# Kernel optimization log

Hardware: AMD Instinct MI355X
Metric: run time of the kernel (lower is better)

The kernel has to match this reference:

```python
import jax, jax.numpy as jnp
import numpy as np

B, N, L, E, H, D = 2, 2048, 2048, 512, 8, 3
C = E // H
ALPHA_Q = 10.0

def _ln(v, g, b):
    m = jnp.mean(v, -1, keepdims=True)
    var = jnp.mean((v - m) ** 2, -1, keepdims=True)
    return (v - m) * jax.lax.rsqrt(var + 1e-5) * g + b

def setup_inputs() -> dict:
    key = jax.random.key(0)
    ks = jax.random.split(key, 16)
    def nrm(k, shape):
        return jax.random.normal(k, shape, jnp.float32) * 0.02
    return dict(
        x=jax.random.normal(ks[0], (B, N, E), jnp.float32),
        xp=jax.random.normal(ks[1], (B, N, D), jnp.float32),
        y=jax.random.normal(ks[2], (B, L, E), jnp.float32),
        yp=jax.random.normal(ks[3], (B, L, D), jnp.float32),
        attn_mask=jnp.ones((B, 1, N, L), jnp.float32),
        pW1=jax.random.uniform(ks[4], (E, D), jnp.float32, -1.0 / D, 1.0 / D),
        pb1=jax.random.uniform(ks[5], (E,), jnp.float32, 0.0, np.pi),
        pW2=jax.random.uniform(ks[6], (E, D), jnp.float32, -1.0 / D, 1.0 / D),
        pb2=jax.random.uniform(ks[7], (E,), jnp.float32, 0.0, np.pi),
        qn_g=jnp.ones((E,), jnp.float32), qn_b=jnp.zeros((E,), jnp.float32),
        qW1=nrm(ks[8], (E, E)), qb1=jnp.zeros((E,), jnp.float32),
        qW2=nrm(ks[9], (E, E)), qb2=jnp.zeros((E,), jnp.float32),
        kn_g=jnp.ones((E,), jnp.float32), kn_b=jnp.zeros((E,), jnp.float32),
        kW1=nrm(ks[10], (E, E)), kb1=jnp.zeros((E,), jnp.float32),
        vn_g=jnp.ones((E,), jnp.float32), vn_b=jnp.zeros((E,), jnp.float32),
        vW=nrm(ks[11], (E, E)), vb=jnp.zeros((E,), jnp.float32),
        p1W=nrm(ks[12], (E, E)), p1b=jnp.zeros((E,), jnp.float32),
        p2W=nrm(ks[13], (E, D * H)), p2b=jnp.zeros((E,), jnp.float32),
    )

def reference(x, xp, y, yp, attn_mask, pW1, pb1, pW2, pb2,
              qn_g, qn_b, qW1, qb1, qW2, qb2, kn_g, kn_b, kW1, kb1,
              vn_g, vn_b, vW, vb, p1W, p1b, p2W, p2b):
    # PositionEncoder: query side with bias, key side without
    pxs = ALPHA_Q * xp
    px1 = pxs @ pW1.T + pb1
    px2 = pxs @ pW2.T + pb2
    xc1, xs1, xc2, xs2 = jnp.cos(px1), jnp.sin(px1), jnp.cos(px2), jnp.sin(px2)
    pys = ALPHA_Q * yp
    py1 = pys @ pW1.T
    py2 = pys @ pW2.T
    yc1, ys1, yc2, ys2 = jnp.cos(py1), jnp.sin(py1), jnp.cos(py2), jnp.sin(py2)

    def split(t):  # [B,S,E] -> [B,S,H,C]
        return t.reshape(t.shape[0], t.shape[1], H, C)

    # QueryEncoder
    xn = _ln(x, qn_g, qn_b)
    x1 = xn @ qW1.T + qb1
    x2 = xn @ qW2.T + qb2
    q = jnp.concatenate([split(x1 * xc1), split(x1 * xs1),
                         split(x2 * xc2), split(x2 * xs2)], -1)  # [B,N,H,4C]
    q = q.transpose(0, 2, 1, 3)  # [B,H,N,4C]
    # KeyEncoder
    yn = _ln(y, kn_g, kn_b)
    y1 = yn @ kW1.T + kb1
    k = jnp.concatenate([split(y1 * yc1), split(y1 * ys1),
                         split(yc2), split(ys2)], -1).transpose(0, 2, 1, 3)

    scale = (4 * C) ** -0.5
    attn = jax.nn.softmax(jnp.einsum('bhnd,bhld->bhnl', q, k) * scale, axis=-1)
    # custom mask renormalization
    attn = attn * attn_mask
    eps = min(1e-8, 1.0 / L)
    attn = attn / (jnp.sum(attn, -1, keepdims=True) + eps)

    v = (_ln(y, vn_g, vn_b) @ vW.T + vb).reshape(B, L, H, C).transpose(0, 2, 1, 3)
    out1 = jnp.einsum('bhnl,bhlc->bhnc', attn, v).transpose(0, 2, 1, 3).reshape(B, N, E)
    out1 = out1 @ p1W.T + p1b

    out2 = jnp.einsum('bhnl,bld->bhnd', attn, yp) - xp[:, None]  # [B,H,N,D]
    out2 = out2.transpose(0, 2, 1, 3).reshape(B, N, H * D) @ p2W.T + p2b
    return (out1 + out2, attn)
```

## Files before the change

kernel.cpp:

```cpp
#include <hip/hip_runtime.h>

typedef unsigned short ushort_t;
typedef __attribute__((ext_vector_type(8))) __bf16 bf16x8;
typedef __attribute__((ext_vector_type(4))) float f32x4;

__device__ __forceinline__ f32x4 mfma16(bf16x8 a, bf16x8 b, f32x4 c) {
  return __builtin_amdgcn_mfma_f32_16x16x32_bf16(a, b, c, 0, 0, 0);
}

__device__ __forceinline__ ushort_t f2bf(float f) {
  unsigned int x = __float_as_uint(f);
  unsigned int r = (x + 0x7fffu + ((x >> 16) & 1u)) >> 16;
  return (ushort_t)r;
}

static constexpr size_t SZ_XN   = 4096ull * 512 * 2;
static constexpr size_t SZ_W    = 512ull * 512 * 2;
static constexpr size_t OFS_XN   = 0;
static constexpr size_t OFS_YNK  = OFS_XN + SZ_XN;
static constexpr size_t OFS_YNV  = OFS_YNK + SZ_XN;
static constexpr size_t OFS_WQ12 = OFS_YNV + SZ_XN;
static constexpr size_t OFS_WK1  = OFS_WQ12 + 2 * SZ_W;
static constexpr size_t OFS_WV   = OFS_WK1 + SZ_W;
static constexpr size_t OFS_WP1  = OFS_WV + SZ_W;
static constexpr size_t OFS_QB12 = OFS_WP1 + SZ_W;
static constexpr size_t OFS_FLAG = OFS_QB12 + 4096;
static constexpr size_t OFS_X12  = OFS_FLAG + 256;
static constexpr size_t OFS_INV  = OFS_X12;
static constexpr size_t OFS_Y1   = OFS_X12 + 4096ull * 1024 * 4;
static constexpr size_t OFS_VV   = OFS_Y1 + 4096ull * 512 * 4;
static constexpr size_t OFS_Q    = OFS_VV + 4096ull * 512 * 4;
static constexpr size_t OFS_K    = OFS_Q + 16ull * 2048 * 256 * 2;
static constexpr size_t OFS_VT   = OFS_K + 16ull * 2048 * 256 * 2;
static constexpr size_t OFS_O1   = OFS_VT + 16ull * 80 * 2048 * 2;
static constexpr size_t OFS_O2   = OFS_O1 + 4096ull * 512 * 2;
static constexpr size_t OFS_T    = OFS_O2 + 4096ull * 24 * 4;

__global__ void k_convert(const float* __restrict__ qW1, const float* __restrict__ qW2,
                          const float* __restrict__ kW1, const float* __restrict__ vW,
                          const float* __restrict__ p1W,
                          const float* __restrict__ qb1, const float* __restrict__ qb2,
                          ushort_t* wq12, ushort_t* wk1, ushort_t* wv, ushort_t* wp1,
                          float* qb12, int* flag) {
  int seg = blockIdx.y;
  int idx = blockIdx.x * 256 + threadIdx.x;
  switch (seg) {
    case 0: wq12[idx] = f2bf(qW1[idx]);
            if (idx < 512) qb12[idx] = qb1[idx];
            if (idx == 0) *flag = 1;
            break;
    case 1: wq12[262144 + idx] = f2bf(qW2[idx]);
            if (idx < 512) qb12[512 + idx] = qb2[idx];
            break;
    case 2: wk1[idx] = f2bf(kW1[idx]); break;
    case 3: wv[idx]  = f2bf(vW[idx]);  break;
    case 4: wp1[idx] = f2bf(p1W[idx]); break;
  }
}

__global__ void k_maskchk(const float4* __restrict__ mask, int* flag, int n4) {
  int i = blockIdx.x * blockDim.x + threadIdx.x;
  bool bad = false;
  for (; i < n4; i += gridDim.x * blockDim.x) {
    float4 v = mask[i];
    bad |= (v.x != 1.f) | (v.y != 1.f) | (v.z != 1.f) | (v.w != 1.f);
  }
  if (bad) atomicAnd(flag, 0);
}

__global__ __launch_bounds__(256) void k_ln1(const float* __restrict__ x,
                                             const float* __restrict__ g, const float* __restrict__ b,
                                             ushort_t* __restrict__ out) {
  int row = blockIdx.x, tid = threadIdx.x;
  const float* xr = x + (size_t)row * 512;
  float v0 = xr[tid], v1 = xr[tid + 256];
  float s = v0 + v1, q = v0 * v0 + v1 * v1;
  for (int m = 32; m; m >>= 1) { s += __shfl_xor(s, m, 64); q += __shfl_xor(q, m, 64); }
  __shared__ float ls[8];
  int wid = tid >> 6, lane = tid & 63;
  if (lane == 0) { ls[wid] = s; ls[4 + wid] = q; }
  __syncthreads();
  s = ls[0] + ls[1] + ls[2] + ls[3];
  q = ls[4] + ls[5] + ls[6] + ls[7];
  float mean = s * (1.f / 512), var = q * (1.f / 512) - mean * mean;
  float rs = rsqrtf(var + 1e-5f);
  ushort_t* o = out + (size_t)row * 512;
  o[tid]       = f2bf((v0 - mean) * rs * g[tid] + b[tid]);
  o[tid + 256] = f2bf((v1 - mean) * rs * g[tid + 256] + b[tid + 256]);
}

__global__ __launch_bounds__(256) void k_ln2(const float* __restrict__ y,
                                             const float* __restrict__ g1, const float* __restrict__ b1,
                                             const float* __restrict__ g2, const float* __restrict__ b2,
                                             ushort_t* __restrict__ o1, ushort_t* __restrict__ o2) {
  int row = blockIdx.x, tid = threadIdx.x;
  const float* yr = y + (size_t)row * 512;
  float v0 = yr[tid], v1 = yr[tid + 256];
  float s = v0 + v1, q = v0 * v0 + v1 * v1;
  for (int m = 32; m; m >>= 1) { s += __shfl_xor(s, m, 64); q += __shfl_xor(q, m, 64); }
  __shared__ float ls[8];
  int wid = tid >> 6, lane = tid & 63;
  if (lane == 0) { ls[wid] = s; ls[4 + wid] = q; }
  __syncthreads();
  s = ls[0] + ls[1] + ls[2] + ls[3];
  q = ls[4] + ls[5] + ls[6] + ls[7];
  float mean = s * (1.f / 512), var = q * (1.f / 512) - mean * mean;
  float rs = rsqrtf(var + 1e-5f);
  float t0 = (v0 - mean) * rs, t1 = (v1 - mean) * rs;
  ushort_t* p1 = o1 + (size_t)row * 512;
  ushort_t* p2 = o2 + (size_t)row * 512;
  p1[tid]       = f2bf(t0 * g1[tid] + b1[tid]);
  p1[tid + 256] = f2bf(t1 * g1[tid + 256] + b1[tid + 256]);
  p2[tid]       = f2bf(t0 * g2[tid] + b2[tid]);
  p2[tid + 256] = f2bf(t1 * g2[tid + 256] + b2[tid + 256]);
}

__global__ __launch_bounds__(256) void k_gemm(const ushort_t* __restrict__ A, const ushort_t* __restrict__ W,
                                              const float* __restrict__ bias, float* __restrict__ Cmat,
                                              int M, int Nn, int K, int mode,
                                              const float* __restrict__ o2, const float* __restrict__ p2W,
                                              const float* __restrict__ p2b) {
  __shared__ __align__(16) ushort_t lA[128 * 40];
  __shared__ __align__(16) ushort_t lB[128 * 40];
  int tid = threadIdx.x;
  int wid = tid >> 6, lane = tid & 63, lg = lane >> 4, lc = lane & 15;
  int m0 = blockIdx.y * 128, n0 = blockIdx.x * 128;
  int wm = wid >> 1, wn = wid & 1;
  f32x4 acc[4][4];
#pragma unroll
  for (int i = 0; i < 4; i++)
#pragma unroll
    for (int j = 0; j < 4; j++) acc[i][j] = (f32x4){0, 0, 0, 0};

  for (int k0 = 0; k0 < K; k0 += 32) {
    __syncthreads();
#pragma unroll
    for (int i = 0; i < 2; i++) {
      int u = tid + i * 256;
      int row = u >> 2, off = u & 3;
      *(int4*)(&lA[row * 40 + off * 8]) = *(const int4*)(A + (size_t)(m0 + row) * K + k0 + off * 8);
      *(int4*)(&lB[row * 40 + off * 8]) = *(const int4*)(W + (size_t)(n0 + row) * K + k0 + off * 8);
    }
    __syncthreads();
    bf16x8 af[4], bf[4];
#pragma unroll
    for (int mt = 0; mt < 4; mt++) af[mt] = *(const bf16x8*)(&lA[(wm * 64 + mt * 16 + lc) * 40 + lg * 8]);
#pragma unroll
    for (int nt = 0; nt < 4; nt++) bf[nt] = *(const bf16x8*)(&lB[(wn * 64 + nt * 16 + lc) * 40 + lg * 8]);
#pragma unroll
    for (int mt = 0; mt < 4; mt++)
#pragma unroll
      for (int nt = 0; nt < 4; nt++) acc[mt][nt] = mfma16(af[mt], bf[nt], acc[mt][nt]);
  }

#pragma unroll
  for (int mt = 0; mt < 4; mt++) {
#pragma unroll
    for (int nt = 0; nt < 4; nt++) {
      int col = n0 + wn * 64 + nt * 16 + lc;
      float bcol = bias[col];
#pragma unroll
      for (int r = 0; r < 4; r++) {
        int row = m0 + wm * 64 + mt * 16 + lg * 4 + r;
        float v = acc[mt][nt][r] + bcol;
        if (mode == 1) {
          const float* o2r = o2 + (size_t)row * 24;
          const float* wr = p2W + (size_t)col * 24;
          float sdot = p2b[col];
#pragma unroll
          for (int j = 0; j < 24; j++) sdot += o2r[j] * wr[j];
          v += sdot;
        }
        Cmat[(size_t)row * Nn + col] = v;
      }
    }
  }
}

__global__ __launch_bounds__(256) void k_scatter_q(const float* __restrict__ x12, const float* __restrict__ xp,
                                                   const float* __restrict__ pW1, const float* __restrict__ pb1,
                                                   const float* __restrict__ pW2, const float* __restrict__ pb2,
                                                   ushort_t* __restrict__ q) {
  int rown = blockIdx.x;
  int b = rown >> 11, n = rown & 2047;
  float p0 = xp[(size_t)rown * 3] * 10.f;
  float p1 = xp[(size_t)rown * 3 + 1] * 10.f;
  float p2v = xp[(size_t)rown * 3 + 2] * 10.f;
  const float* x1r = x12 + (size_t)rown * 1024;
#pragma unroll
  for (int i = 0; i < 2; i++) {
    int e = threadIdx.x + i * 256;
    float a1 = p0 * pW1[e * 3] + p1 * pW1[e * 3 + 1] + p2v * pW1[e * 3 + 2] + pb1[e];
    float a2 = p0 * pW2[e * 3] + p1 * pW2[e * 3 + 1] + p2v * pW2[e * 3 + 2] + pb2[e];
    float c1, s1, c2, s2;
    __sincosf(a1, &s1, &c1);
    __sincosf(a2, &s2, &c2);
    float x1 = x1r[e], x2 = x1r[512 + e];
    int h = e >> 6, c = e & 63;
    ushort_t* qr = q + (((size_t)b * 8 + h) * 2048 + n) * 256;
    qr[c]       = f2bf(x1 * c1);
    qr[64 + c]  = f2bf(x1 * s1);
    qr[128 + c] = f2bf(x2 * c2);
    qr[192 + c] = f2bf(x2 * s2);
  }
}

__global__ __launch_bounds__(256) void k_scatter_k(const float* __restrict__ y1, const float* __restrict__ yp,
                                                   const float* __restrict__ pW1, const float* __restrict__ pW2,
                                                   ushort_t* __restrict__ kk) {
  int rown = blockIdx.x;
  int b = rown >> 11, n = rown & 2047;
  float p0 = yp[(size_t)rown * 3] * 10.f;
  float p1 = yp[(size_t)rown * 3 + 1] * 10.f;
  float p2v = yp[(size_t)rown * 3 + 2] * 10.f;
  const float* y1r = y1 + (size_t)rown * 512;
#pragma unroll
  for (int i = 0; i < 2; i++) {
    int e = threadIdx.x + i * 256;
    float a1 = p0 * pW1[e * 3] + p1 * pW1[e * 3 + 1] + p2v * pW1[e * 3 + 2];
    float a2 = p0 * pW2[e * 3] + p1 * pW2[e * 3 + 1] + p2v * pW2[e * 3 + 2];
    float c1, s1, c2, s2;
    __sincosf(a1, &s1, &c1);
    __sincosf(a2, &s2, &c2);
    float v1 = y1r[e];
    int h = e >> 6, c = e & 63;
    ushort_t* kr = kk + (((size_t)b * 8 + h) * 2048 + n) * 256;
    kr[c]       = f2bf(v1 * c1);
    kr[64 + c]  = f2bf(v1 * s1);
    kr[128 + c] = f2bf(c2);
    kr[192 + c] = f2bf(s2);
  }
}

__global__ void k_vt(const float* __restrict__ vv, ushort_t* __restrict__ vt) {
  int l0 = blockIdx.x * 64, h = blockIdx.y, b = blockIdx.z;
  __shared__ ushort_t t[64][66];
  int tx = threadIdx.x, ty = threadIdx.y;
#pragma unroll
  for (int i = 0; i < 16; i++) {
    int lr = i * 4 + ty;
    t[lr][tx] = f2bf(vv[((size_t)(b * 2048 + l0 + lr)) * 512 + h * 64 + tx]);
  }
  __syncthreads();
#pragma unroll
  for (int i = 0; i < 16; i++) {
    int col = i * 4 + ty;
    vt[(((size_t)b * 8 + h) * 80 + col) * 2048 + l0 + tx] = t[tx][col];
  }
}

__global__ void k_vt_extra(const float* __restrict__ yp, ushort_t* __restrict__ vt) {
  int l = blockIdx.x * 256 + threadIdx.x;
  int j = blockIdx.y, bh = blockIdx.z;
  int b = bh >> 3;
  ushort_t v = 0;
  if (j < 3) v = f2bf(yp[((size_t)b * 2048 + l) * 3 + j]);
  vt[((size_t)bh * 80 + 64 + j) * 2048 + l] = v;
}

__global__ __launch_bounds__(256, 2) void k_attn1(const ushort_t* __restrict__ qbuf,
                                                  const ushort_t* __restrict__ kbuf,
                                                  const ushort_t* __restrict__ vt,
                                                  const float* __restrict__ mask,
                                                  const int* __restrict__ flag,
                                                  const float* __restrict__ xp,
                                                  float* __restrict__ invb,
                                                  ushort_t* __restrict__ Tb,
                                                  ushort_t* __restrict__ o1,
                                                  float* __restrict__ o2) {
  __shared__ __align__(16) ushort_t kL[2][32 * 256];
  __shared__ __align__(16) ushort_t aT[4][16][40];

  int flat = blockIdx.x;
  int bh = flat & 15, rb = flat >> 4;
  int b = bh >> 3, h = bh & 7;
  int tid = threadIdx.x, wid = tid >> 6, lane = tid & 63, lg = lane >> 4, lc = lane & 15;
  int wrow = rb * 64 + wid * 16;
  const bool ones = (*flag != 0);

  const ushort_t* Kb = kbuf + (size_t)bh * 2048 * 256;
  const ushort_t* Vb = vt + (size_t)bh * 80 * 2048;
  ushort_t* Trow = Tb + ((size_t)bh * 2048 + wrow + lc) * 2048 + lg * 8;

  bf16x8 qf[8];
  {
    const ushort_t* qr = qbuf + ((size_t)bh * 2048 + wrow + lc) * 256 + lg * 8;
#pragma unroll
    for (int ks = 0; ks < 8; ks++) qf[ks] = *(const bf16x8*)(qr + ks * 32);
  }

  int sg_src[4], sg_dst[4];
#pragma unroll
  for (int i = 0; i < 4; i++) {
    int g = wid * 256 + i * 64 + lane;
    int row = g >> 5;
    int gc = (g & 31) ^ (row & 7);
    sg_src[i] = row * 256 + gc * 8;
    sg_dst[i] = (wid * 256 + i * 64) * 8;
  }

#define STAGE(s, t)                                                                     \
  {                                                                                     \
    const ushort_t* tb = Kb + (size_t)(t) * 32 * 256;                                   \
    _Pragma("unroll")                                                                   \
    for (int i = 0; i < 4; i++) {                                                       \
      __builtin_amdgcn_global_load_lds(                                                 \
          (const __attribute__((address_space(1))) void*)(tb + sg_src[i]),              \
          (__attribute__((address_space(3))) void*)(&kL[s][sg_dst[i]]), 16, 0, 0);      \
    }                                                                                   \
  }

  int r3 = (lc & 7);

  float rsE[4] = {0, 0, 0, 0}, rsM[4] = {0, 0, 0, 0};
  f32x4 pacc[5];
#pragma unroll
  for (int nt = 0; nt < 5; nt++) pacc[nt] = (f32x4){0, 0, 0, 0};

  STAGE(0, 0);
  asm volatile("s_waitcnt vmcnt(0)" ::: "memory");
  __builtin_amdgcn_s_barrier();
  __builtin_amdgcn_sched_barrier(0);

  for (int t = 0; t < 64; t++) {
    int s = t & 1;
    int l0 = t * 32;
    if (t < 63) { STAGE(s ^ 1, t + 1); }
    bf16x8 vf[5];
#pragma unroll
    for (int nt = 0; nt < 5; nt++)
      vf[nt] = *(const bf16x8*)(Vb + (size_t)(nt * 16 + lc) * 2048 + l0 + lg * 8);
    __builtin_amdgcn_sched_barrier(0);
    f32x4 sacc[2];
    sacc[0] = (f32x4){0, 0, 0, 0};
    sacc[1] = (f32x4){0, 0, 0, 0};
#pragma unroll
    for (int ks = 0; ks < 8; ks++) {
      int gb = ((ks * 4 + lg) ^ r3) * 8;
      bf16x8 k0 = *(const bf16x8*)(&kL[s][lc * 256 + gb]);
      bf16x8 k1 = *(const bf16x8*)(&kL[s][(16 + lc) * 256 + gb]);
      sacc[0] = mfma16(qf[ks], k0, sacc[0]);
      sacc[1] = mfma16(qf[ks], k1, sacc[1]);
    }
#pragma unroll
    for (int nt = 0; nt < 2; nt++)
#pragma unroll
      for (int r = 0; r < 4; r++) {
        float T = __expf(sacc[nt][r] * 0.0625f);
        rsE[r] += T;
        float Tm = T;
        if (!ones) {
          float m = mask[((size_t)b * 2048 + wrow + lg * 4 + r) * 2048 + l0 + nt * 16 + lc];
          Tm = T * m;
          rsM[r] += Tm;
        }
        aT[wid][lg * 4 + r][nt * 16 + lc] = f2bf(Tm);
      }
    asm volatile("s_waitcnt lgkmcnt(0)" ::: "memory");
    __builtin_amdgcn_sched_barrier(0);
    bf16x8 af = *(const bf16x8*)(&aT[wid][lc][lg * 8]);
    *(bf16x8*)(Trow + l0) = af;
#pragma unroll
    for (int nt = 0; nt < 5; nt++) pacc[nt] = mfma16(af, vf[nt], pacc[nt]);
    asm volatile("s_waitcnt vmcnt(1)" ::: "memory");
    __builtin_amdgcn_s_barrier();
    __builtin_amdgcn_sched_barrier(0);
  }
#undef STAGE

  float inv[4];
#pragma unroll
  for (int r = 0; r < 4; r++) {
#pragma unroll
    for (int s2 = 1; s2 < 16; s2 <<= 1) {
      rsE[r] += __shfl_xor(rsE[r], s2, 64);
      if (!ones) rsM[r] += __shfl_xor(rsM[r], s2, 64);
    }
    float denom = (ones ? rsE[r] : rsM[r]) + 1e-8f * rsE[r];
    inv[r] = 1.f / denom;
  }
  if (lc == 0) {
#pragma unroll
    for (int r = 0; r < 4; r++) invb[(size_t)bh * 2048 + wrow + lg * 4 + r] = inv[r];
  }

#pragma unroll
  for (int nt = 0; nt < 4; nt++)
#pragma unroll
    for (int r = 0; r < 4; r++) {
      int n = wrow + lg * 4 + r;
      o1[((size_t)b * 2048 + n) * 512 + h * 64 + nt * 16 + lc] = f2bf(pacc[nt][r] * inv[r]);
    }
  if (lc < 3) {
#pragma unroll
    for (int r = 0; r < 4; r++) {
      int n = wrow + lg * 4 + r;
      o2[((size_t)b * 2048 + n) * 24 + h * 3 + lc] =
          pacc[4][r] * inv[r] - xp[((size_t)b * 2048 + n) * 3 + lc];
    }
  }
}

__global__ __launch_bounds__(256) void k_norm(const ushort_t* __restrict__ Tb,
                                              const float* __restrict__ invb,
                                              float* __restrict__ attn_out) {
  int tid = threadIdx.x;
  size_t rowbase = (size_t)blockIdx.x * 8;
#pragma unroll
  for (int rr = 0; rr < 8; rr++) {
    size_t row = rowbase + rr;
    float inv = invb[row];
    const ushort_t* src = Tb + row * 2048 + tid * 8;
    float* dst = attn_out + row * 2048 + tid * 8;
    int4 v = *(const int4*)src;
    const unsigned* u = (const unsigned*)&v;
    f32x4 f0, f1;
#pragma unroll
    for (int j = 0; j < 2; j++) {
      f0[2 * j]     = __uint_as_float(u[j] << 16) * inv;
      f0[2 * j + 1] = __uint_as_float(u[j] & 0xffff0000u) * inv;
      f1[2 * j]     = __uint_as_float(u[2 + j] << 16) * inv;
      f1[2 * j + 1] = __uint_as_float(u[2 + j] & 0xffff0000u) * inv;
    }
    __builtin_nontemporal_store(f0, (f32x4*)dst);
    __builtin_nontemporal_store(f1, (f32x4*)(dst + 4));
  }
}

extern "C" void kernel_launch(void* const* d_in, const int* in_sizes, int n_in,
                              void* d_out, int out_size, void* d_ws, size_t ws_size,
                              hipStream_t stream) {
  const float* x    = (const float*)d_in[0];
  const float* xp   = (const float*)d_in[1];
  const float* y    = (const float*)d_in[2];
  const float* yp   = (const float*)d_in[3];
  const float* mask = (const float*)d_in[4];
  const float* pW1  = (const float*)d_in[5];
  const float* pb1  = (const float*)d_in[6];
  const float* pW2  = (const float*)d_in[7];
  const float* pb2  = (const float*)d_in[8];
  const float* qn_g = (const float*)d_in[9];
  const float* qn_b = (const float*)d_in[10];
  const float* qW1  = (const float*)d_in[11];
  const float* qb1  = (const float*)d_in[12];
  const float* qW2  = (const float*)d_in[13];
  const float* qb2  = (const float*)d_in[14];
  const float* kn_g = (const float*)d_in[15];
  const float* kn_b = (const float*)d_in[16];
  const float* kW1  = (const float*)d_in[17];
  const float* kb1  = (const float*)d_in[18];
  const float* vn_g = (const float*)d_in[19];
  const float* vn_b = (const float*)d_in[20];
  const float* vW   = (const float*)d_in[21];
  const float* vb   = (const float*)d_in[22];
  const float* p1W  = (const float*)d_in[23];
  const float* p1b  = (const float*)d_in[24];
  const float* p2W  = (const float*)d_in[25];
  const float* p2b  = (const float*)d_in[26];

  char* ws = (char*)d_ws;
  ushort_t* xn   = (ushort_t*)(ws + OFS_XN);
  ushort_t* ynk  = (ushort_t*)(ws + OFS_YNK);
  ushort_t* ynv  = (ushort_t*)(ws + OFS_YNV);
  ushort_t* wq12 = (ushort_t*)(ws + OFS_WQ12);
  ushort_t* wk1  = (ushort_t*)(ws + OFS_WK1);
  ushort_t* wv   = (ushort_t*)(ws + OFS_WV);
  ushort_t* wp1  = (ushort_t*)(ws + OFS_WP1);
  float*    qb12 = (float*)(ws + OFS_QB12);
  int*      flag = (int*)(ws + OFS_FLAG);
  float*    x12  = (float*)(ws + OFS_X12);
  float*    invb = (float*)(ws + OFS_INV);
  float*    y1b  = (float*)(ws + OFS_Y1);
  float*    vvb  = (float*)(ws + OFS_VV);
  ushort_t* qb   = (ushort_t*)(ws + OFS_Q);
  ushort_t* kb   = (ushort_t*)(ws + OFS_K);
  ushort_t* vtb  = (ushort_t*)(ws + OFS_VT);
  ushort_t* o1   = (ushort_t*)(ws + OFS_O1);
  float*    o2   = (float*)(ws + OFS_O2);
  ushort_t* Tb   = (ushort_t*)(ws + OFS_T);

  float* out0 = (float*)d_out;
  float* attn_out = (float*)d_out + 2097152;

  k_convert<<<dim3(1024, 5), 256, 0, stream>>>(qW1, qW2, kW1, vW, p1W, qb1, qb2,
                                               wq12, wk1, wv, wp1, qb12, flag);
  k_maskchk<<<2048, 256, 0, stream>>>((const float4*)mask, flag, 2097152);
  k_ln1<<<4096, 256, 0, stream>>>(x, qn_g, qn_b, xn);
  k_ln2<<<4096, 256, 0, stream>>>(y, kn_g, kn_b, vn_g, vn_b, ynk, ynv);
  k_gemm<<<dim3(8, 32), 256, 0, stream>>>(xn, wq12, qb12, x12, 4096, 1024, 512, 0, nullptr, nullptr, nullptr);
  k_gemm<<<dim3(4, 32), 256, 0, stream>>>(ynk, wk1, kb1, y1b, 4096, 512, 512, 0, nullptr, nullptr, nullptr);
  k_gemm<<<dim3(4, 32), 256, 0, stream>>>(ynv, wv, vb, vvb, 4096, 512, 512, 0, nullptr, nullptr, nullptr);
  k_scatter_q<<<4096, 256, 0, stream>>>(x12, xp, pW1, pb1, pW2, pb2, qb);
  k_scatter_k<<<4096, 256, 0, stream>>>(y1b, yp, pW1, pW2, kb);
  k_vt<<<dim3(32, 8, 2), dim3(64, 4), 0, stream>>>(vvb, vtb);
  k_vt_extra<<<dim3(8, 16, 16), 256, 0, stream>>>(yp, vtb);
  k_attn1<<<dim3(512), 256, 0, stream>>>(qb, kb, vtb, mask, flag, xp, invb, Tb, o1, o2);
  k_gemm<<<dim3(4, 32), 256, 0, stream>>>(o1, wp1, p1b, out0, 4096, 512, 512, 1, o2, p2W, p2b);
  k_norm<<<dim3(4096), 256, 0, stream>>>(Tb, invb, attn_out);
}
```

Measured before the change: 366.7 us.

## Split P@V out of attention kernel and fuse it with attn normalization

The attention kernel now only computes QK^T scores, exp, row sums and the unnormalized bf16 probability tile, and its K staging moves from double to triple buffering so loads run two tiles ahead. The P@V product (including the yp extra columns) moves into a new k_pv kernel. That kernel re-reads the bf16 probability tile, writes the normalized fp32 attention output, and accumulates P@V with the L dimension split across warps, reduced in shared memory. This removes V loads and extra MFMAs from the hot attention loop and folds the separate normalization pass into the P@V pass. The cost is an extra launch, a cross-warp reduction, and a larger LDS footprint in the attention kernel.

```diff
diff --git a/kernel.cpp b/kernel.cpp
--- a/kernel.cpp
+++ b/kernel.cpp
@@ -3,6 +3,7 @@
 typedef unsigned short ushort_t;
 typedef __attribute__((ext_vector_type(8))) __bf16 bf16x8;
 typedef __attribute__((ext_vector_type(4))) float f32x4;
+typedef __attribute__((ext_vector_type(4))) int i32x4;
 
 __device__ __forceinline__ f32x4 mfma16(bf16x8 a, bf16x8 b, f32x4 c) {
   return __builtin_amdgcn_mfma_f32_16x16x32_bf16(a, b, c, 0, 0, 0);
@@ -260,26 +261,21 @@
 
 __global__ __launch_bounds__(256, 2) void k_attn1(const ushort_t* __restrict__ qbuf,
                                                   const ushort_t* __restrict__ kbuf,
-                                                  const ushort_t* __restrict__ vt,
                                                   const float* __restrict__ mask,
                                                   const int* __restrict__ flag,
-                                                  const float* __restrict__ xp,
                                                   float* __restrict__ invb,
-                                                  ushort_t* __restrict__ Tb,
-                                                  ushort_t* __restrict__ o1,
-                                                  float* __restrict__ o2) {
-  __shared__ __align__(16) ushort_t kL[2][32 * 256];
+                                                  ushort_t* __restrict__ Tb) {
+  __shared__ __align__(16) ushort_t kL[3][32 * 256];
   __shared__ __align__(16) ushort_t aT[4][16][40];
 
   int flat = blockIdx.x;
   int bh = flat & 15, rb = flat >> 4;
-  int b = bh >> 3, h = bh & 7;
+  int b = bh >> 3;
   int tid = threadIdx.x, wid = tid >> 6, lane = tid & 63, lg = lane >> 4, lc = lane & 15;
   int wrow = rb * 64 + wid * 16;
   const bool ones = (*flag != 0);
 
   const ushort_t* Kb = kbuf + (size_t)bh * 2048 * 256;
-  const ushort_t* Vb = vt + (size_t)bh * 80 * 2048;
   ushort_t* Trow = Tb + ((size_t)bh * 2048 + wrow + lc) * 2048 + lg * 8;
 
   bf16x8 qf[8];
@@ -313,32 +309,28 @@
   int r3 = (lc & 7);
 
   float rsE[4] = {0, 0, 0, 0}, rsM[4] = {0, 0, 0, 0};
-  f32x4 pacc[5];
-#pragma unroll
-  for (int nt = 0; nt < 5; nt++) pacc[nt] = (f32x4){0, 0, 0, 0};
 
   STAGE(0, 0);
-  asm volatile("s_waitcnt vmcnt(0)" ::: "memory");
+  STAGE(1, 1);
+  asm volatile("s_waitcnt vmcnt(4)" ::: "memory");
   __builtin_amdgcn_s_barrier();
   __builtin_amdgcn_sched_barrier(0);
 
+  int cur = 0;
   for (int t = 0; t < 64; t++) {
-    int s = t & 1;
     int l0 = t * 32;
-    if (t < 63) { STAGE(s ^ 1, t + 1); }
-    bf16x8 vf[5];
-#pragma unroll
-    for (int nt = 0; nt < 5; nt++)
-      vf[nt] = *(const bf16x8*)(Vb + (size_t)(nt * 16 + lc) * 2048 + l0 + lg * 8);
+    int st = cur + 2; if (st >= 3) st -= 3;
+    if (t + 2 < 64) { STAGE(st, t + 2); }
     __builtin_amdgcn_sched_barrier(0);
     f32x4 sacc[2];
     sacc[0] = (f32x4){0, 0, 0, 0};
     sacc[1] = (f32x4){0, 0, 0, 0};
+    const ushort_t* kc = &kL[cur][0];
 #pragma unroll
     for (int ks = 0; ks < 8; ks++) {
       int gb = ((ks * 4 + lg) ^ r3) * 8;
-      bf16x8 k0 = *(const bf16x8*)(&kL[s][lc * 256 + gb]);
-      bf16x8 k1 = *(const bf16x8*)(&kL[s][(16 + lc) * 256 + gb]);
+      bf16x8 k0 = *(const bf16x8*)(kc + lc * 256 + gb);
+      bf16x8 k1 = *(const bf16x8*)(kc + (16 + lc) * 256 + gb);
       sacc[0] = mfma16(qf[ks], k0, sacc[0]);
       sacc[1] = mfma16(qf[ks], k1, sacc[1]);
     }
@@ -359,12 +351,14 @@
     asm volatile("s_waitcnt lgkmcnt(0)" ::: "memory");
     __builtin_amdgcn_sched_barrier(0);
     bf16x8 af = *(const bf16x8*)(&aT[wid][lc][lg * 8]);
-    *(bf16x8*)(Trow + l0) = af;
-#pragma unroll
-    for (int nt = 0; nt < 5; nt++) pacc[nt] = mfma16(af, vf[nt], pacc[nt]);
-    asm volatile("s_waitcnt vmcnt(1)" ::: "memory");
-    __builtin_amdgcn_s_barrier();
-    __builtin_amdgcn_sched_barrier(0);
+    __builtin_nontemporal_store(*(const i32x4*)&af, (i32x4*)(Trow + l0));
+    if (t < 63) {
+      if (t + 2 < 64) { asm volatile("s_waitcnt vmcnt(6)" ::: "memory"); }
+      else            { asm volatile("s_waitcnt vmcnt(2)" ::: "memory"); }
+      __builtin_amdgcn_s_barrier();
+      __builtin_amdgcn_sched_barrier(0);
+    }
+    cur = (cur + 1 == 3) ? 0 : cur + 1;
   }
 #undef STAGE
 
@@ -383,47 +377,74 @@
 #pragma unroll
     for (int r = 0; r < 4; r++) invb[(size_t)bh * 2048 + wrow + lg * 4 + r] = inv[r];
   }
-
-#pragma unroll
-  for (int nt = 0; nt < 4; nt++)
-#pragma unroll
-    for (int r = 0; r < 4; r++) {
-      int n = wrow + lg * 4 + r;
-      o1[((size_t)b * 2048 + n) * 512 + h * 64 + nt * 16 + lc] = f2bf(pacc[nt][r] * inv[r]);
-    }
-  if (lc < 3) {
-#pragma unroll
-    for (int r = 0; r < 4; r++) {
-      int n = wrow + lg * 4 + r;
-      o2[((size_t)b * 2048 + n) * 24 + h * 3 + lc] =
-          pacc[4][r] * inv[r] - xp[((size_t)b * 2048 + n) * 3 + lc];
-    }
-  }
-}
-
-__global__ __launch_bounds__(256) void k_norm(const ushort_t* __restrict__ Tb,
-                                              const float* __restrict__ invb,
-                                              float* __restrict__ attn_out) {
-  int tid = threadIdx.x;
-  size_t rowbase = (size_t)blockIdx.x * 8;
-#pragma unroll
-  for (int rr = 0; rr < 8; rr++) {
-    size_t row = rowbase + rr;
-    float inv = invb[row];
-    const ushort_t* src = Tb + row * 2048 + tid * 8;
-    float* dst = attn_out + row * 2048 + tid * 8;
-    int4 v = *(const int4*)src;
-    const unsigned* u = (const unsigned*)&v;
+}
+
+__global__ __launch_bounds__(256) void k_pv(const ushort_t* __restrict__ Tb,
+                                            const ushort_t* __restrict__ vt,
+                                            const float* __restrict__ invb,
+                                            const float* __restrict__ xp,
+                                            float* __restrict__ attn_out,
+                                            ushort_t* __restrict__ o1,
+                                            float* __restrict__ o2) {
+  __shared__ float red[4][16][80];
+  int blk = blockIdx.x;
+  int bh = blk & 15, mb = blk >> 4;
+  int b = bh >> 3, h = bh & 7;
+  int m0 = mb * 16;
+  int tid = threadIdx.x, wid = tid >> 6, lane = tid & 63, lg = lane >> 4, lc = lane & 15;
+
+  const ushort_t* Trow = Tb + ((size_t)bh * 2048 + m0 + lc) * 2048 + lg * 8;
+  float* arow = attn_out + ((size_t)bh * 2048 + m0 + lc) * 2048 + lg * 8;
+  const ushort_t* Vb = vt + (size_t)bh * 80 * 2048;
+  float invr = invb[(size_t)bh * 2048 + m0 + lc];
+
+  f32x4 pacc[5];
+#pragma unroll
+  for (int nt = 0; nt < 5; nt++) pacc[nt] = (f32x4){0, 0, 0, 0};
+
+  int lbase = wid * 512;
+  for (int it = 0; it < 16; it++) {
+    int l0 = lbase + it * 32;
+    i32x4 ub = __builtin_nontemporal_load((const i32x4*)(Trow + l0));
+    bf16x8 af = *(const bf16x8*)&ub;
+    const unsigned* u = (const unsigned*)&ub;
     f32x4 f0, f1;
 #pragma unroll
     for (int j = 0; j < 2; j++) {
-      f0[2 * j]     = __uint_as_float(u[j] << 16) * inv;
-      f0[2 * j + 1] = __uint_as_float(u[j] & 0xffff0000u) * inv;
-      f1[2 * j]     = __uint_as_float(u[2 + j] << 16) * inv;
-      f1[2 * j + 1] = __uint_as_float(u[2 + j] & 0xffff0000u) * inv;
-    }
-    __builtin_nontemporal_store(f0, (f32x4*)dst);
-    __builtin_nontemporal_store(f1, (f32x4*)(dst + 4));
+      f0[2 * j]     = __uint_as_float(u[j] << 16) * invr;
+      f0[2 * j + 1] = __uint_as_float(u[j] & 0xffff0000u) * invr;
+      f1[2 * j]     = __uint_as_float(u[2 + j] << 16) * invr;
+      f1[2 * j + 1] = __uint_as_float(u[2 + j] & 0xffff0000u) * invr;
+    }
+    __builtin_nontemporal_store(f0, (f32x4*)(arow + l0));
+    __builtin_nontemporal_store(f1, (f32x4*)(arow + l0 + 4));
+#pragma unroll
+    for (int nt = 0; nt < 5; nt++) {
+      bf16x8 vf = *(const bf16x8*)(Vb + (size_t)(nt * 16 + lc) * 2048 + l0 + lg * 8);
+      pacc[nt] = mfma16(af, vf, pacc[nt]);
+    }
+  }
+
+#pragma unroll
+  for (int nt = 0; nt < 5; nt++)
+#pragma unroll
+    for (int r = 0; r < 4; r++) red[wid][lg * 4 + r][nt * 16 + lc] = pacc[nt][r];
+  __syncthreads();
+
+#pragma unroll
+  for (int j = 0; j < 5; j++) {
+    int e = tid + j * 256;
+    int row = e / 80, col = e - row * 80;
+    float s = red[0][row][col] + red[1][row][col] + red[2][row][col] + red[3][row][col];
+    float iv = invb[(size_t)bh * 2048 + m0 + row];
+    float sv = s * iv;
+    size_t gr = (size_t)b * 2048 + m0 + row;
+    if (col < 64) {
+      o1[gr * 512 + h * 64 + col] = f2bf(sv);
+    } else if (col < 67) {
+      int j2 = col - 64;
+      o2[gr * 24 + h * 3 + j2] = sv - xp[gr * 3 + j2];
+    }
   }
 }
 
@@ -494,7 +515,7 @@
   k_scatter_k<<<4096, 256, 0, stream>>>(y1b, yp, pW1, pW2, kb);
   k_vt<<<dim3(32, 8, 2), dim3(64, 4), 0, stream>>>(vvb, vtb);
   k_vt_extra<<<dim3(8, 16, 16), 256, 0, stream>>>(yp, vtb);
-  k_attn1<<<dim3(512), 256, 0, stream>>>(qb, kb, vtb, mask, flag, xp, invb, Tb, o1, o2);
+  k_attn1<<<dim3(512), 256, 0, stream>>>(qb, kb, mask, flag, invb, Tb);
+  k_pv<<<dim3(2048), 256, 0, stream>>>(Tb, vtb, invb, xp, attn_out, o1, o2);
   k_gemm<<<dim3(4, 32), 256, 0, stream>>>(o1, wp1, p1b, out0, 4096, 512, 512, 1, o2, p2W, p2b);
-  k_norm<<<dim3(4096), 256, 0, stream>>>(Tb, invb, attn_out);
-}
+}
```

After: 399.9 us. 9.1% more time.

## Triple-buffer K tiles, batch Tb stores per four tiles, re-grid norm kernel

Applied to the files above, without the earlier changes.

The attention kernel moves from double to triple buffering of K tiles in LDS, issuing loads two tiles ahead so the global-to-LDS transfers overlap more compute. Unnormalised probabilities are now held in a wider LDS scratch covering four tiles and written to the Tb buffer every fourth iteration as 64-byte contiguous row segments with nontemporal stores, replacing one 16-byte store per lane per tile. The normalisation kernel is re-gridded to one wave per row with nontemporal loads. The cost is more LDS per block, which could limit occupancy, plus tighter wait-count bookkeeping.

```diff
diff --git a/kernel.cpp b/kernel.cpp
--- a/kernel.cpp
+++ b/kernel.cpp
@@ -3,6 +3,7 @@
 typedef unsigned short ushort_t;
 typedef __attribute__((ext_vector_type(8))) __bf16 bf16x8;
 typedef __attribute__((ext_vector_type(4))) float f32x4;
+typedef __attribute__((ext_vector_type(4))) int i32x4;
 
 __device__ __forceinline__ f32x4 mfma16(bf16x8 a, bf16x8 b, f32x4 c) {
   return __builtin_amdgcn_mfma_f32_16x16x32_bf16(a, b, c, 0, 0, 0);
@@ -268,8 +269,8 @@
                                                   ushort_t* __restrict__ Tb,
                                                   ushort_t* __restrict__ o1,
                                                   float* __restrict__ o2) {
-  __shared__ __align__(16) ushort_t kL[2][32 * 256];
-  __shared__ __align__(16) ushort_t aT[4][16][40];
+  __shared__ __align__(16) ushort_t kL[3][32 * 256];
+  __shared__ __align__(16) ushort_t aT[4][16][136];
 
   int flat = blockIdx.x;
   int bh = flat & 15, rb = flat >> 4;
@@ -280,7 +281,6 @@
 
   const ushort_t* Kb = kbuf + (size_t)bh * 2048 * 256;
   const ushort_t* Vb = vt + (size_t)bh * 80 * 2048;
-  ushort_t* Trow = Tb + ((size_t)bh * 2048 + wrow + lc) * 2048 + lg * 8;
 
   bf16x8 qf[8];
   {
@@ -311,6 +311,8 @@
   }
 
   int r3 = (lc & 7);
+  int srr = lane >> 2, scq = (lane & 3) * 32;
+  ushort_t* Tst = Tb + ((size_t)bh * 2048 + wrow + srr) * 2048 + scq;
 
   float rsE[4] = {0, 0, 0, 0}, rsM[4] = {0, 0, 0, 0};
   f32x4 pacc[5];
@@ -318,27 +320,33 @@
   for (int nt = 0; nt < 5; nt++) pacc[nt] = (f32x4){0, 0, 0, 0};
 
   STAGE(0, 0);
-  asm volatile("s_waitcnt vmcnt(0)" ::: "memory");
+  STAGE(1, 1);
+  asm volatile("s_waitcnt vmcnt(4)" ::: "memory");
   __builtin_amdgcn_s_barrier();
   __builtin_amdgcn_sched_barrier(0);
 
+  int cur = 0;
   for (int t = 0; t < 64; t++) {
-    int s = t & 1;
     int l0 = t * 32;
-    if (t < 63) { STAGE(s ^ 1, t + 1); }
+    int p = t & 3;
     bf16x8 vf[5];
 #pragma unroll
     for (int nt = 0; nt < 5; nt++)
       vf[nt] = *(const bf16x8*)(Vb + (size_t)(nt * 16 + lc) * 2048 + l0 + lg * 8);
     __builtin_amdgcn_sched_barrier(0);
+    int st = cur + 2; if (st >= 3) st -= 3;
+    if (t + 2 < 64) { STAGE(st, t + 2); }
+    __builtin_amdgcn_sched_barrier(0);
+
     f32x4 sacc[2];
     sacc[0] = (f32x4){0, 0, 0, 0};
     sacc[1] = (f32x4){0, 0, 0, 0};
+    const ushort_t* kc = &kL[cur][0];
 #pragma unroll
     for (int ks = 0; ks < 8; ks++) {
       int gb = ((ks * 4 + lg) ^ r3) * 8;
-      bf16x8 k0 = *(const bf16x8*)(&kL[s][lc * 256 + gb]);
-      bf16x8 k1 = *(const bf16x8*)(&kL[s][(16 + lc) * 256 + gb]);
+      bf16x8 k0 = *(const bf16x8*)(kc + lc * 256 + gb);
+      bf16x8 k1 = *(const bf16x8*)(kc + (16 + lc) * 256 + gb);
       sacc[0] = mfma16(qf[ks], k0, sacc[0]);
       sacc[1] = mfma16(qf[ks], k1, sacc[1]);
     }
@@ -354,17 +362,26 @@
           Tm = T * m;
           rsM[r] += Tm;
         }
-        aT[wid][lg * 4 + r][nt * 16 + lc] = f2bf(Tm);
+        aT[wid][lg * 4 + r][p * 32 + nt * 16 + lc] = f2bf(Tm);
       }
     asm volatile("s_waitcnt lgkmcnt(0)" ::: "memory");
     __builtin_amdgcn_sched_barrier(0);
-    bf16x8 af = *(const bf16x8*)(&aT[wid][lc][lg * 8]);
-    *(bf16x8*)(Trow + l0) = af;
+    bf16x8 af = *(const bf16x8*)(&aT[wid][lc][p * 32 + lg * 8]);
 #pragma unroll
     for (int nt = 0; nt < 5; nt++) pacc[nt] = mfma16(af, vf[nt], pacc[nt]);
-    asm volatile("s_waitcnt vmcnt(1)" ::: "memory");
+
+    if (p == 3) {
+      int c0 = l0 - 96;
+#pragma unroll
+      for (int j = 0; j < 4; j++) {
+        bf16x8 av = *(const bf16x8*)(&aT[wid][srr][scq + j * 8]);
+        __builtin_nontemporal_store(*(const i32x4*)&av, (i32x4*)(Tst + c0 + j * 8));
+      }
+    }
+    __builtin_amdgcn_sched_barrier(0);
     __builtin_amdgcn_s_barrier();
     __builtin_amdgcn_sched_barrier(0);
+    cur = (cur + 1 == 3) ? 0 : cur + 1;
   }
 #undef STAGE
 
@@ -404,15 +421,15 @@
 __global__ __launch_bounds__(256) void k_norm(const ushort_t* __restrict__ Tb,
                                               const float* __restrict__ invb,
                                               float* __restrict__ attn_out) {
-  int tid = threadIdx.x;
-  size_t rowbase = (size_t)blockIdx.x * 8;
-#pragma unroll
-  for (int rr = 0; rr < 8; rr++) {
-    size_t row = rowbase + rr;
-    float inv = invb[row];
-    const ushort_t* src = Tb + row * 2048 + tid * 8;
-    float* dst = attn_out + row * 2048 + tid * 8;
-    int4 v = *(const int4*)src;
+  int wid = threadIdx.x >> 6, lane = threadIdx.x & 63;
+  size_t row = (size_t)blockIdx.x * 4 + wid;
+  float inv = invb[row];
+  const ushort_t* src = Tb + row * 2048;
+  float* dst = attn_out + row * 2048;
+#pragma unroll
+  for (int c = 0; c < 4; c++) {
+    int off = c * 512 + lane * 8;
+    i32x4 v = __builtin_nontemporal_load((const i32x4*)(src + off));
     const unsigned* u = (const unsigned*)&v;
     f32x4 f0, f1;
 #pragma unroll
@@ -422,8 +439,8 @@
       f1[2 * j]     = __uint_as_float(u[2 + j] << 16) * inv;
       f1[2 * j + 1] = __uint_as_float(u[2 + j] & 0xffff0000u) * inv;
     }
-    __builtin_nontemporal_store(f0, (f32x4*)dst);
-    __builtin_nontemporal_store(f1, (f32x4*)(dst + 4));
+    __builtin_nontemporal_store(f0, (f32x4*)(dst + off));
+    __builtin_nontemporal_store(f1, (f32x4*)(dst + off + 4));
   }
 }
 
@@ -496,5 +513,5 @@
   k_vt_extra<<<dim3(8, 16, 16), 256, 0, stream>>>(yp, vtb);
   k_attn1<<<dim3(512), 256, 0, stream>>>(qb, kb, vtb, mask, flag, xp, invb, Tb, o1, o2);
   k_gemm<<<dim3(4, 32), 256, 0, stream>>>(o1, wp1, p1b, out0, 4096, 512, 512, 1, o2, p2W, p2b);
-  k_norm<<<dim3(4096), 256, 0, stream>>>(Tb, invb, attn_out);
-}
+  k_norm<<<dim3(8192), 256, 0, stream>>>(Tb, invb, attn_out);
+}
```

After: 473.3 us. 1.29x slower.
